# Optimization experiments

Hardware: AMD Instinct MI355X
Metric: run time of the kernel (lower is better)

The kernel has to match this reference:

```python
import jax, jax.numpy as jnp
import numpy as np

B, T, D = 1, 1024, 1024
H = 16; HKV = 16; HD = D // H; R = 2; K = 3; LOWR = 32
HR = HKV * R                      # heads after harmonic expansion
OUTW = HKV * HD * 2 * R           # w_proj output width
SCALE = HD ** -0.5


def setup_inputs() -> dict:
    key = jax.random.key(0)
    ks = jax.random.split(key, 10)
    def rn(k, shape, sc=1.0):
        return jax.random.normal(k, shape, dtype=jnp.float32) * sc
    return {
        'hidden_states': rn(ks[0], (B, T, D)),
        'q_w': rn(ks[1], (D, D), D ** -0.5),
        'k_w': rn(ks[2], (D, D), D ** -0.5),
        'v_w': rn(ks[3], (D, D), D ** -0.5),
        'w1': rn(ks[4], (LOWR, D), D ** -0.5),
        'w2': rn(ks[5], (OUTW, LOWR), LOWR ** -0.5),
        'conv_w': rn(ks[6], (OUTW, K), K ** -0.5),
        'bt_w': rn(ks[7], (HKV * R, D), D ** -0.5),
        'bt_b': jnp.zeros((HKV * R,), jnp.float32),
        'o_w': rn(ks[8], (D, D * R), (D * R) ** -0.5),
        'omega': 0.01 * jnp.ones((1, 1, 1, R), jnp.float32),
        'phi': jnp.zeros((1, 1, 1, R), jnp.float32),
    }


def path_attention_forward(hidden_states, q_w, k_w, v_w, w1, w2, conv_w,
                           bt_w, bt_b, o_w, omega, phi):
    b, t, _ = hidden_states.shape
    q = hidden_states @ q_w.T
    k = hidden_states @ k_w.T
    v = hidden_states @ v_w.T
    # low-rank w projection, causal depthwise short conv (kernel K), SiLU
    w_raw = (hidden_states @ w1.T) @ w2.T                    # [b,t,OUTW]
    xp = jnp.pad(w_raw, ((0, 0), (K - 1, 0), (0, 0)))
    w_raw = sum(xp[:, i:i + t, :] * conv_w[:, i] for i in range(K))
    w_raw = jax.nn.silu(w_raw)
    # rotary-like harmonic mixing of Householder directions
    w5 = w_raw.reshape(b, t, HKV, 2 * R, HD)
    Ah = w5[:, :, :, 0::2, :]                                # [b,t,HKV,R,HD]
    Bh = w5[:, :, :, 1::2, :]
    pos = jnp.arange(t, dtype=jnp.float32)[None, :, None, None]
    theta = omega * pos + phi                                # [1,t,1,R]
    c = jnp.cos(theta)[..., None]
    s = jnp.sin(theta)[..., None]
    Wdir = Ah * c + Bh * s
    Wdir = Wdir * jax.lax.rsqrt(jnp.sum(Wdir * Wdir, -1, keepdims=True) + 1e-6)
    beta = jax.nn.sigmoid(hidden_states @ bt_w.T + bt_b) * 2.0   # [b,t,HR]
    # repeat-interleave q/k/v heads across harmonics -> [b,HR,t,HD]
    to_h = lambda x: jnp.swapaxes(jnp.repeat(x.reshape(b, t, H, HD), R, axis=2), 1, 2)
    qh, kh, vh = to_h(q), to_h(k), to_h(v)
    wh = jnp.swapaxes(Wdir.reshape(b, t, HR, HD), 1, 2)      # [b,HR,t,HD]
    bh = jnp.swapaxes(beta, 1, 2)                            # [b,HR,t]
    # PaTH logits: A_ij = q_i^T (H_i ... H_{j+1}) k_j, H_t = I - beta_t w_t w_t^T.
    # WY/UT transform: with M_ts = beta_t (w_t.w_s) for s<t, the coefficients
    # B_tj (t>j) of the accumulated rank-1 corrections solve the unit-lower
    # triangular system (I + M) B = strilow(Db W K^T), and
    # A = tril(Q K^T - tril(Q W^T) B).
    idx = jnp.arange(t)
    strict = idx[:, None] > idx[None, :]
    incl = idx[:, None] >= idx[None, :]
    Mw = jnp.where(strict, jnp.einsum('bhtd,bhsd->bhts', wh, wh) * bh[..., None], 0.0)
    rhs = jnp.where(strict, jnp.einsum('bhtd,bhjd->bhtj', wh, kh) * bh[..., None], 0.0)
    Bmat = jax.scipy.linalg.solve_triangular(Mw + jnp.eye(t, dtype=Mw.dtype), rhs, lower=True)
    qk = jnp.einsum('bhid,bhjd->bhij', qh, kh)
    qw = jnp.where(incl, jnp.einsum('bhid,bhtd->bhit', qh, wh), 0.0)
    logits = (qk - jnp.einsum('bhit,bhtj->bhij', qw, Bmat)) * SCALE
    logits = jnp.where(incl, logits, -1e30)
    p = jax.nn.softmax(logits, axis=-1)
    o = jnp.einsum('bhij,bhjd->bhid', p, vh)                 # [b,HR,t,HD]
    o = jnp.swapaxes(o, 1, 2).reshape(b, t, HR * HD)         # [b,t,D*R]
    return o @ o_w.T


def reference(hidden_states, q_w, k_w, v_w, w1, w2, conv_w, bt_w, bt_b, o_w, omega, phi):
    return path_attention_forward(hidden_states, q_w, k_w, v_w, w1, w2, conv_w,
                                  bt_w, bt_b, o_w, omega, phi)
```

## Files before the change

### kernel.cpp

```cpp
#include <hip/hip_runtime.h>
#include <math.h>

#define TTD 1024
#define DDM 1024
#define HDIM 64
#define PSC2 0.18033688011112042f
#define LS 72

typedef __attribute__((ext_vector_type(8))) __bf16 bf16x8;
typedef __attribute__((ext_vector_type(4))) float f32x4;
#define MFMA16(a,b,c) __builtin_amdgcn_mfma_f32_16x16x32_bf16(a,b,c,0,0,0)

#define STR_(x) #x
#define WAITVM(N) asm volatile("s_waitcnt vmcnt(" STR_(N) ")" ::: "memory")
#define BAR() do { __builtin_amdgcn_s_barrier(); asm volatile("" ::: "memory"); } while (0)
#define LGKBAR() do { asm volatile("s_waitcnt lgkmcnt(0)" ::: "memory"); \
                      __builtin_amdgcn_s_barrier(); asm volatile("" ::: "memory"); } while (0)
#define FULLBAR() do { asm volatile("s_waitcnt vmcnt(0) lgkmcnt(0)" ::: "memory"); \
                       __builtin_amdgcn_s_barrier(); asm volatile("" ::: "memory"); } while (0)

__device__ __forceinline__ ushort f2b(float f) {
  unsigned u = __builtin_bit_cast(unsigned, f);
  return (ushort)((u + 0x7fffu + ((u >> 16) & 1u)) >> 16);
}
__device__ __forceinline__ float b2f(ushort u) {
  unsigned v = (unsigned)u << 16;
  return __builtin_bit_cast(float, v);
}

__device__ __forceinline__ void gload_lds16(const ushort* g, ushort* l) {
  __builtin_amdgcn_global_load_lds(
      (const __attribute__((address_space(1))) unsigned*)g,
      (__attribute__((address_space(3))) unsigned*)l, 16, 0, 0);
}

#define SWZ(row, cc) (((row) * 8 + ((cc) ^ ((row) & 7))) * 8)
#define SWZE(row, col) (SWZ(row, (col) >> 3) + ((col) & 7))
#define SWZ2(row, cc) (((row) * 8 + ((cc) ^ (((row) & 7) ^ ((row) >> 3)))) * 8)
#define SWZ2E(row, col) (SWZ2(row, (col) >> 3) + ((col) & 7))

__device__ __forceinline__ void stage_tile(const ushort* gb, long gs, ushort* tile,
                                           int w, int l) {
  int sub = l >> 3, cc = (l & 7) ^ sub;
  #pragma unroll
  for (int it = 0; it < 2; ++it) {
    int q = w * 2 + it;
    gload_lds16(gb + (long)(q * 8 + sub) * gs + cc * 8, &tile[(q * 64 + l) * 8]);
  }
}

__device__ __forceinline__ bf16x8 frag(const ushort* tile, int row, int cc) {
  return *(const bf16x8*)&tile[SWZ(row, cc)];
}
__device__ __forceinline__ bf16x8 frag2(const ushort* tile, int row, int cc) {
  return *(const bf16x8*)&tile[SWZ2(row, cc)];
}

#define XT_PERH   557056L
#define OFF_X     0L
#define OFF_PZ    35651584L
#define OFF_HSB   35651584L
#define OFF_QWW   37748736L
#define OFF_KWW   39845888L
#define OFF_VWW   41943040L
#define OFF_W2B   44040192L
#define OFF_WLOWB 44302336L
#define OFF_TB    98566144L
#define OFF_OALL  98566144L
#define OFF_YB    102760448L
#define OFF_OWB   106954752L
#define OFF_WHB   111149056L
#define OFF_QB    115343360L
#define OFF_KB    117440512L
#define OFF_VTB   119537664L
#define OFF_BETA  121634816L
#define OFF_BW64  121765888L
#define OFF_PO    121896960L
#define OFF_PML   138674176L

#define CVT_TOTAL 6488064L
struct CvtSegs {
  const float* src[8];
  ushort* dst[8];
  long cnt[8];
};
__global__ __launch_bounds__(256) void cvt_all_kernel(CvtSegs sg) {
  long e = ((long)blockIdx.x * 256 + threadIdx.x) * 4;
  #pragma unroll
  for (int s = 0; s < 8; ++s) {
    if (e < sg.cnt[s]) {
      float4 f = *(const float4*)(sg.src[s] + e);
      ushort4 o;
      o.x = f2b(f.x); o.y = f2b(f.y); o.z = f2b(f.z); o.w = f2b(f.w);
      *(ushort4*)(sg.dst[s] + e) = o;
      return;
    }
    e -= sg.cnt[s];
  }
}

__global__ __launch_bounds__(256) void qkv_sp_kernel(
    const ushort* __restrict__ hsb,
    const ushort* __restrict__ wq, const ushort* __restrict__ wk, const ushort* __restrict__ wv,
    const ushort* __restrict__ bw, const float* __restrict__ bt_b,
    ushort* __restrict__ cq, ushort* __restrict__ ck, ushort* __restrict__ cv,
    float* __restrict__ beta, ushort* __restrict__ wlowb)
{
  int z = blockIdx.z;
  if (z == 3 && blockIdx.x != 0) return;
  const ushort* B = (z == 0) ? wq : (z == 1) ? wk : (z == 2) ? wv : bw;

  __shared__ ushort Ab[2][8192];
  __shared__ ushort Bb[2][4096];

  int tid = threadIdx.x, w = tid >> 6, l = tid & 63;
  int quad = l >> 4, lane15 = l & 15;
  int rm = blockIdx.y * 128, cn = (z == 3) ? 0 : blockIdx.x * 64;
  const ushort* Ag = hsb + (long)rm * DDM;
  const ushort* Bg = B + (long)cn * DDM;

  stage_tile(Ag, DDM, &Ab[0][0], w, l);
  stage_tile(Ag + 64 * DDM, DDM, &Ab[0][4096], w, l);
  stage_tile(Bg, DDM, &Bb[0][0], w, l);

  f32x4 acc[2][4] = {};
  int arow0 = (w & 1) * 32 + lane15;
  int asel = (w >> 1) * 4096;
  for (int kt = 0; kt < 16; ++kt) {
    int cur = kt & 1;
    if (kt < 15) {
      int nxt = cur ^ 1;
      stage_tile(Ag + (kt + 1) * 64, DDM, &Ab[nxt][0], w, l);
      stage_tile(Ag + 64 * DDM + (kt + 1) * 64, DDM, &Ab[nxt][4096], w, l);
      stage_tile(Bg + (kt + 1) * 64, DDM, &Bb[nxt][0], w, l);
      WAITVM(6);
    } else {
      WAITVM(0);
    }
    BAR();
    const ushort* Atile = &Ab[cur][asel];
    #pragma unroll
    for (int s = 0; s < 2; ++s) {
      bf16x8 a0 = frag(Atile, arow0, s * 4 + quad);
      bf16x8 a1 = frag(Atile, arow0 + 16, s * 4 + quad);
      #pragma unroll
      for (int f = 0; f < 4; ++f) {
        bf16x8 bf = frag(&Bb[cur][0], f * 16 + lane15, s * 4 + quad);
        acc[0][f] = MFMA16(a0, bf, acc[0][f]);
        acc[1][f] = MFMA16(a1, bf, acc[1][f]);
      }
    }
    BAR();
  }

  if (z < 2) {
    ushort* Cb = (z == 0) ? cq : ck;
    #pragma unroll
    for (int rr = 0; rr < 2; ++rr) {
      int orow = rm + w * 32 + rr * 16 + quad * 4;
      #pragma unroll
      for (int f = 0; f < 4; ++f)
        #pragma unroll
        for (int r = 0; r < 4; ++r)
          Cb[(long)(orow + r) * DDM + cn + f * 16 + lane15] = f2b(acc[rr][f][r]);
    }
  } else if (z == 2) {
    #pragma unroll
    for (int rr = 0; rr < 2; ++rr) {
      int orow = rm + w * 32 + rr * 16 + quad * 4;
      #pragma unroll
      for (int f = 0; f < 4; ++f) {
        ushort4 o;
        o.x = f2b(acc[rr][f][0]); o.y = f2b(acc[rr][f][1]);
        o.z = f2b(acc[rr][f][2]); o.w = f2b(acc[rr][f][3]);
        *(ushort4*)&cv[(long)(cn + f * 16 + lane15) * TTD + orow] = o;
      }
    }
  } else {
    #pragma unroll
    for (int rr = 0; rr < 2; ++rr) {
      int orow = rm + w * 32 + rr * 16 + quad * 4;
      #pragma unroll
      for (int f = 0; f < 2; ++f) {
        int hr = f * 16 + lane15;
        float bb = bt_b[hr];
        #pragma unroll
        for (int r = 0; r < 4; ++r)
          beta[(long)hr * TTD + orow + r] = 2.f / (1.f + __expf(-(acc[rr][f][r] + bb)));
      }
      #pragma unroll
      for (int f = 2; f < 4; ++f)
        #pragma unroll
        for (int r = 0; r < 4; ++r)
          wlowb[(long)(orow + r) * 32 + (f - 2) * 16 + lane15] = f2b(acc[rr][f][r]);
    }
  }
}

__global__ __launch_bounds__(256) void wraw_solveA_kernel(
    const ushort* __restrict__ wlowb, const ushort* __restrict__ w2b,
    const float* __restrict__ conv_w, const float* __restrict__ omega,
    const float* __restrict__ phi, const float* __restrict__ beta,
    ushort* __restrict__ whb, ushort* __restrict__ TB, ushort* __restrict__ YB)
{
  int c = blockIdx.x;
  int rm = c * 64;
  int p = blockIdx.y;
  int hkv = p >> 1, r = p & 1;
  int c0 = hkv * 256 + r * 128;

  __shared__ char pool_[65568];
  ushort* As = (ushort*)pool_;
  ushort* Bs = (ushort*)(pool_ + 4096);
  float (*WR)[132] = (float(*)[132])(pool_ + 12288);
  ushort* Wrow = (ushort*)(pool_ + 47136);
  ushort* WT   = (ushort*)(pool_ + 56352);
  float (*Lm)[65] = (float(*)[65])pool_;
  float (*Vf)[65] = (float(*)[65])(pool_ + 16640);
  ushort* Tb = (ushort*)(pool_ + 33280);

  int tid = threadIdx.x, w = tid >> 6, l = tid & 63;
  int quad = l >> 4, lane15 = l & 15;

  {
    int row = tid >> 2, ch = (tid & 3) * 8;
    gload_lds16(wlowb + (long)(rm + row) * 32 + ch, &As[row * 32 + ch]);
    gload_lds16(w2b + (long)(c0 + row) * 32 + ch, &Bs[row * 32 + ch]);
    gload_lds16(w2b + (long)(c0 + 64 + row) * 32 + ch, &Bs[(64 + row) * 32 + ch]);
  }
  {
    int hr2 = tid >> 7, col = tid & 127;
    float acc = 0.f;
    if (rm > 0) {
      long t = rm - 2 + hr2;
      for (int k = 0; k < 32; ++k)
        acc += b2f(wlowb[t * 32 + k]) * b2f(w2b[(long)(c0 + col) * 32 + k]);
    }
    WR[hr2][col] = acc;
  }
  FULLBAR();

  #pragma unroll
  for (int g = 0; g < 2; ++g) {
    f32x4 acc[4] = {};
    bf16x8 af = *(const bf16x8*)&As[(w * 16 + lane15) * 32 + quad * 8];
    #pragma unroll
    for (int f = 0; f < 4; ++f) {
      bf16x8 bf = *(const bf16x8*)&Bs[(g * 64 + f * 16 + lane15) * 32 + quad * 8];
      acc[f] = MFMA16(af, bf, acc[f]);
    }
    #pragma unroll
    for (int f = 0; f < 4; ++f)
      #pragma unroll
      for (int rr = 0; rr < 4; ++rr)
        WR[2 + w * 16 + quad * 4 + rr][g * 64 + f * 16 + lane15] = acc[f][rr];
  }
  LGKBAR();

  {
    float cwa[3], cwb[3];
    #pragma unroll
    for (int i = 0; i < 3; ++i) {
      cwa[i] = conv_w[(long)(c0 + l) * 3 + i];
      cwb[i] = conv_w[(long)(c0 + 64 + l) * 3 + i];
    }
    float om = omega[r], ph = phi[r];
    for (int it = 0; it < 16; ++it) {
      int tl = it * 4 + w;
      int t = rm + tl;
      float a = cwa[0] * WR[tl][l] + cwa[1] * WR[tl + 1][l] + cwa[2] * WR[tl + 2][l];
      float b = cwb[0] * WR[tl][64 + l] + cwb[1] * WR[tl + 1][64 + l] + cwb[2] * WR[tl + 2][64 + l];
      a = a / (1.f + __expf(-a));
      b = b / (1.f + __expf(-b));
      float th = om * (float)t + ph;
      float wd = a * __cosf(th) + b * __sinf(th);
      float ss = wd * wd;
      #pragma unroll
      for (int o = 32; o > 0; o >>= 1) ss += __shfl_xor(ss, o, 64);
      ushort hv = f2b(wd * (1.f / sqrtf(ss + 1e-6f)));
      whb[((long)p * TTD + t) * HDIM + l] = hv;
      Wrow[tl * LS + l] = hv;
      WT[l * LS + tl] = hv;
    }
  }
  LGKBAR();

  const float* bet = beta + (long)p * TTD + rm;
  ushort* TBh = TB + ((long)p * 16 + c) * 4096;
  ushort* YBh = YB + ((long)p * 16 + c) * 4096;

  f32x4 g4[4] = {};
  #pragma unroll
  for (int s = 0; s < 2; ++s) {
    bf16x8 af = *(const bf16x8*)&Wrow[(w * 16 + lane15) * LS + s * 32 + quad * 8];
    #pragma unroll
    for (int f = 0; f < 4; ++f) {
      bf16x8 bf = *(const bf16x8*)&Wrow[(f * 16 + lane15) * LS + s * 32 + quad * 8];
      g4[f] = MFMA16(af, bf, g4[f]);
    }
  }
  #pragma unroll
  for (int r4 = 0; r4 < 4; ++r4) {
    int t = w * 16 + quad * 4 + r4;
    float bv = bet[t];
    #pragma unroll
    for (int f = 0; f < 4; ++f) {
      int tp = f * 16 + lane15;
      Lm[t][tp] = (t > tp) ? bv * g4[f][r4] : 0.f;
    }
  }
  LGKBAR();

  {
    float cur[16];
    #pragma unroll
    for (int i = 0; i < 16; ++i) cur[i] = (w * 16 + i == l) ? bet[l] : 0.f;
    for (int sb = 0; sb < 4; ++sb) {
      if (w == sb) {
        float xloc[16];
        #pragma unroll
        for (int i = 0; i < 16; ++i) {
          float bv = cur[i];
          #pragma unroll
          for (int j2 = 0; j2 < 16; ++j2)
            if (j2 < i) bv -= Lm[sb * 16 + i][sb * 16 + j2] * xloc[j2];
          xloc[i] = bv;
          Vf[sb * 16 + i][l] = bv;
        }
      }
      LGKBAR();
      if (w > sb) {
        float xp[16];
        #pragma unroll
        for (int t = 0; t < 16; ++t) xp[t] = Vf[sb * 16 + t][l];
        #pragma unroll
        for (int i = 0; i < 16; ++i) {
          float s2 = cur[i];
          #pragma unroll
          for (int t = 0; t < 16; ++t) s2 -= Lm[w * 16 + i][sb * 16 + t] * xp[t];
          cur[i] = s2;
        }
      }
    }
  }
  {
    int t = tid >> 2, off = (tid & 3) * 16;
    ushort tmp[16];
    #pragma unroll
    for (int i = 0; i < 16; ++i) { tmp[i] = f2b(Vf[t][off + i]); Tb[t * LS + off + i] = tmp[i]; }
    *(uint4*)&TBh[t * 64 + off] = *(const uint4*)&tmp[0];
    *(uint4*)&TBh[t * 64 + off + 8] = *(const uint4*)&tmp[8];
  }
  LGKBAR();
  f32x4 y[4] = {};
  #pragma unroll
  for (int s = 0; s < 2; ++s) {
    bf16x8 af = *(const bf16x8*)&Tb[(w * 16 + lane15) * LS + s * 32 + quad * 8];
    #pragma unroll
    for (int f = 0; f < 4; ++f) {
      bf16x8 bf = *(const bf16x8*)&WT[(f * 16 + lane15) * LS + s * 32 + quad * 8];
      y[f] = MFMA16(af, bf, y[f]);
    }
  }
  #pragma unroll
  for (int f = 0; f < 4; ++f)
    #pragma unroll
    for (int r4 = 0; r4 < 4; ++r4)
      YBh[(long)(w * 16 + quad * 4 + r4) * 64 + f * 16 + lane15] = f2b(y[f][r4]);
}

__global__ __launch_bounds__(256) void solveB_kernel(
    const ushort* __restrict__ whb, const ushort* __restrict__ kb,
    const ushort* __restrict__ TB, const ushort* __restrict__ YB,
    ushort* __restrict__ Xb, ushort* __restrict__ KZ)
{
  int h = blockIdx.x;
  int ty = blockIdx.y;
  int js = (ty < 8) ? ty : (23 - ty);
  int j0 = js * 64;
  const ushort* wh_h = whb + (long)h * TTD * HDIM;
  const ushort* k_h = kb + (long)(h >> 1) * 64;
  ushort* X_h = Xb + (long)h * XT_PERH;
  ushort* KZ_h = KZ + (long)h * 15 * TTD * HDIM;
  int xidx = js * 16 - js * (js - 1) / 2;

  __shared__ ushort KT[4096];
  __shared__ ushort WT[4096];
  __shared__ ushort XM[4096];
  __shared__ ushort nS[4096];

  int tid = threadIdx.x, w = tid >> 6, l = tid & 63;
  int quad = l >> 4, lane15 = l & 15;
  f32x4 Sacc[4] = {}, Wacc[4] = {};

  stage_tile(k_h + (long)j0 * DDM, DDM, KT, w, l);

  float kreg[4][4];
  #pragma unroll
  for (int f = 0; f < 4; ++f)
    #pragma unroll
    for (int r = 0; r < 4; ++r)
      kreg[f][r] = b2f(k_h[(long)(j0 + w * 16 + quad * 4 + r) * DDM + f * 16 + lane15]);

  int prow0 = tid >> 3, pd0 = (tid & 7) * 8;
  uint4 pk0 = *(const uint4*)&wh_h[((long)js * 64 + prow0) * HDIM + pd0];
  uint4 pk1 = *(const uint4*)&wh_h[((long)js * 64 + 32 + prow0) * HDIM + pd0];
  bf16x8 ybr0 = {}, ybr1 = {};

  WAITVM(0);

  for (int c = js; c < 16; ++c) {
    LGKBAR();
    {
      const ushort* pu0 = (const ushort*)&pk0;
      const ushort* pu1 = (const ushort*)&pk1;
      #pragma unroll
      for (int i = 0; i < 8; ++i) WT[SWZ2E(pd0 + i, prow0)] = pu0[i];
      #pragma unroll
      for (int i = 0; i < 8; ++i) WT[SWZ2E(pd0 + i, 32 + prow0)] = pu1[i];
    }
    if (c < 15) {
      pk0 = *(const uint4*)&wh_h[((long)(c + 1) * 64 + prow0) * HDIM + pd0];
      pk1 = *(const uint4*)&wh_h[((long)(c + 1) * 64 + 32 + prow0) * HDIM + pd0];
    }
    f32x4 xacc[4] = {};
    if (c == js) {
      const ushort* whc = wh_h + (long)c * 64 * HDIM;
      f32x4 m[4] = {};
      #pragma unroll
      for (int s = 0; s < 2; ++s) {
        bf16x8 af = *(const bf16x8*)&whc[(long)(w * 16 + lane15) * HDIM + s * 32 + quad * 8];
        #pragma unroll
        for (int f = 0; f < 4; ++f)
          m[f] = MFMA16(af, frag(KT, f * 16 + lane15, s * 4 + quad), m[f]);
      }
      #pragma unroll
      for (int f = 0; f < 4; ++f)
        #pragma unroll
        for (int r = 0; r < 4; ++r) {
          int t = w * 16 + quad * 4 + r, j = f * 16 + lane15;
          XM[SWZE(j, t)] = (t > j) ? f2b(m[f][r]) : (ushort)0;
        }
      LGKBAR();
      const ushort* TBh = TB + ((long)h * 16 + c) * 4096;
      #pragma unroll
      for (int s = 0; s < 2; ++s) {
        bf16x8 af = *(const bf16x8*)&TBh[(long)(w * 16 + lane15) * 64 + s * 32 + quad * 8];
        #pragma unroll
        for (int f = 0; f < 4; ++f)
          xacc[f] = MFMA16(af, frag(XM, f * 16 + lane15, s * 4 + quad), xacc[f]);
      }
      LGKBAR();
    } else {
      #pragma unroll
      for (int f = 0; f < 4; ++f) {
        xacc[f] = MFMA16(ybr0, frag(KT, f * 16 + lane15, 0 * 4 + quad), xacc[f]);
        xacc[f] = MFMA16(ybr0, frag(nS, f * 16 + lane15, 0 * 4 + quad), xacc[f]);
        xacc[f] = MFMA16(ybr1, frag(KT, f * 16 + lane15, 1 * 4 + quad), xacc[f]);
        xacc[f] = MFMA16(ybr1, frag(nS, f * 16 + lane15, 1 * 4 + quad), xacc[f]);
      }
    }
    #pragma unroll
    for (int f = 0; f < 4; ++f)
      #pragma unroll
      for (int r = 0; r < 4; ++r)
        XM[SWZE(f * 16 + lane15, w * 16 + quad * 4 + r)] = f2b(xacc[f][r]);
    LGKBAR();
    {
      ushort* xt = X_h + (long)xidx * 4096;
      int j = tid >> 2, c2 = (tid & 3) * 2;
      bf16x8 s0 = frag(XM, j, c2);
      bf16x8 s1 = frag(XM, j, c2 + 1);
      *(bf16x8*)&xt[j * 64 + c2 * 8] = s0;
      *(bf16x8*)&xt[j * 64 + c2 * 8 + 8] = s1;
    }
    ++xidx;
    if (c < 15) {
      {
        const ushort* YBn = YB + ((long)h * 16 + c + 1) * 4096;
        ybr0 = *(const bf16x8*)&YBn[(long)(w * 16 + lane15) * 64 + 0 * 32 + quad * 8];
        ybr1 = *(const bf16x8*)&YBn[(long)(w * 16 + lane15) * 64 + 1 * 32 + quad * 8];
      }
      #pragma unroll
      for (int s = 0; s < 2; ++s) {
        bf16x8 aw = frag2(WT, w * 16 + lane15, s * 4 + quad);
        bf16x8 ax = frag(XM, w * 16 + lane15, s * 4 + quad);
        #pragma unroll
        for (int f = 0; f < 4; ++f) {
          Sacc[f] = MFMA16(aw, frag(XM, f * 16 + lane15, s * 4 + quad), Sacc[f]);
          Wacc[f] = MFMA16(ax, frag2(WT, f * 16 + lane15, s * 4 + quad), Wacc[f]);
        }
      }
      ushort* pz = KZ_h + (long)c * TTD * HDIM;
      #pragma unroll
      for (int f = 0; f < 4; ++f)
        #pragma unroll
        for (int r = 0; r < 4; ++r)
          pz[(long)(j0 + w * 16 + quad * 4 + r) * 64 + f * 16 + lane15] =
              f2b(kreg[f][r] - Wacc[f][r]);
      #pragma unroll
      for (int f = 0; f < 4; ++f)
        #pragma unroll
        for (int r = 0; r < 4; ++r)
          nS[SWZE(f * 16 + lane15, w * 16 + quad * 4 + r)] = f2b(-Sacc[f][r]);
    }
  }
}

__global__ __launch_bounds__(256) void flash_kernel(
    const ushort* __restrict__ qb, const ushort* __restrict__ kbuf,
    const ushort* __restrict__ whb, const ushort* __restrict__ Xb,
    const ushort* __restrict__ KZ, const ushort* __restrict__ vTb,
    float* __restrict__ partO, float* __restrict__ partML)
{
  int h = blockIdx.x;
  int y = blockIdx.y;
  int ri = 15 - (y >> 1);
  int half = y & 1;
  int nlo = (ri + 1) >> 1;
  int jb0 = half ? nlo : 0;
  int jb1 = half ? ri : (nlo - 1);
  int r0 = ri * 64;
  const ushort* q_h = qb + (long)(h >> 1) * 64;
  const ushort* k_h = kbuf + (long)(h >> 1) * 64;
  const ushort* wh_h = whb + (long)h * TTD * HDIM;
  const ushort* X_h = Xb + (long)h * XT_PERH;
  const ushort* kz = KZ + ((long)h * 15 + (ri - 1)) * TTD * HDIM;
  const ushort* v_h = vTb + (long)(h >> 1) * 64 * TTD;

  __shared__ ushort S[2][3][4096];
  __shared__ ushort QWD[4096];
  __shared__ ushort PT[4096];

  int tid = threadIdx.x, w = tid >> 6, l = tid & 63;
  int quad = l >> 4, lane15 = l & 15;

  bf16x8 aq[2];
  #pragma unroll
  for (int s = 0; s < 2; ++s)
    aq[s] = *(const bf16x8*)&q_h[(long)(r0 + w * 16 + lane15) * DDM + s * 32 + quad * 8];
  bf16x8 kones;
  #pragma unroll
  for (int i = 0; i < 8; ++i) kones[i] = (__bf16)1.0f;

  long xidx0 = (long)jb0 * 16 - (long)jb0 * (jb0 - 1) / 2 + (ri - jb0);
  const ushort* xst = X_h + xidx0 * 4096;
  if (jb0 <= jb1) {
    if (jb0 == ri) stage_tile(k_h + (long)r0 * DDM, DDM, &S[0][0][0], w, l);
    else           stage_tile(kz + (long)jb0 * 4096, 64, &S[0][0][0], w, l);
    stage_tile(xst, 64, &S[0][1][0], w, l);
    stage_tile(v_h + jb0 * 64, TTD, &S[0][2][0], w, l);
  }
  {
    f32x4 t4[4] = {};
    #pragma unroll
    for (int s = 0; s < 2; ++s)
      #pragma unroll
      for (int f = 0; f < 4; ++f) {
        bf16x8 bf = *(const bf16x8*)&wh_h[(long)(r0 + f * 16 + lane15) * HDIM + s * 32 + quad * 8];
        t4[f] = MFMA16(aq[s], bf, t4[f]);
      }
    #pragma unroll
    for (int f = 0; f < 4; ++f)
      #pragma unroll
      for (int r = 0; r < 4; ++r) {
        int i = w * 16 + quad * 4 + r, t = f * 16 + lane15;
        QWD[SWZE(i, t)] = (i >= t) ? f2b(-t4[f][r]) : (ushort)0;
      }
  }

  f32x4 O[4] = {};
  f32x4 O5 = {};
  float m[4];
  #pragma unroll
  for (int r = 0; r < 4; ++r) m[r] = -1e30f;

  for (int jb = jb0; jb <= jb1; ++jb) {
    int cur = (jb - jb0) & 1;
    const ushort* xnx = xst + (long)(15 - jb) * 4096;
    if (jb < jb1) {
      int jn = jb + 1;
      ushort* nb = &S[cur ^ 1][0][0];
      if (jn < ri) stage_tile(kz + (long)jn * 4096, 64, nb, w, l);
      else         stage_tile(k_h + (long)r0 * DDM, DDM, nb, w, l);
      stage_tile(xnx, 64, nb + 4096, w, l);
      stage_tile(v_h + jn * 64, TTD, nb + 8192, w, l);
      WAITVM(6);
    } else {
      WAITVM(0);
    }
    BAR();
    const ushort* Sb = &S[cur][0][0];
    const ushort* Sx = &S[cur][1][0];
    const ushort* Sv = &S[cur][2][0];
    f32x4 acc[4] = {};
    #pragma unroll
    for (int s = 0; s < 2; ++s)
      #pragma unroll
      for (int f = 0; f < 4; ++f)
        acc[f] = MFMA16(aq[s], frag(Sb, f * 16 + lane15, s * 4 + quad), acc[f]);
    #pragma unroll
    for (int s = 0; s < 2; ++s) {
      bf16x8 aw = frag(QWD, w * 16 + lane15, s * 4 + quad);
      #pragma unroll
      for (int f = 0; f < 4; ++f)
        acc[f] = MFMA16(aw, frag(Sx, f * 16 + lane15, s * 4 + quad), acc[f]);
    }
    float rmax[4] = {-3e38f, -3e38f, -3e38f, -3e38f};
    #pragma unroll
    for (int f = 0; f < 4; ++f)
      #pragma unroll
      for (int r = 0; r < 4; ++r) {
        float lv = acc[f][r] * PSC2;
        if (jb == ri && (f * 16 + lane15) > (w * 16 + quad * 4 + r)) lv = -3e38f;
        acc[f][r] = lv;
        rmax[r] = fmaxf(rmax[r], lv);
      }
    #pragma unroll
    for (int r = 0; r < 4; ++r) {
      rmax[r] = fmaxf(rmax[r], __shfl_xor(rmax[r], 1, 64));
      rmax[r] = fmaxf(rmax[r], __shfl_xor(rmax[r], 2, 64));
      rmax[r] = fmaxf(rmax[r], __shfl_xor(rmax[r], 4, 64));
      rmax[r] = fmaxf(rmax[r], __shfl_xor(rmax[r], 8, 64));
    }
    bool grow = (rmax[0] > m[0]) | (rmax[1] > m[1]) | (rmax[2] > m[2]) | (rmax[3] > m[3]);
    if (__any(grow)) {
      float alpha[4];
      #pragma unroll
      for (int r = 0; r < 4; ++r) {
        float nm = fmaxf(m[r], rmax[r]);
        alpha[r] = exp2f(m[r] - nm);
        m[r] = nm;
        O5[r] *= alpha[r];
      }
      #pragma unroll
      for (int f = 0; f < 4; ++f)
        #pragma unroll
        for (int r = 0; r < 4; ++r) O[f][r] *= alpha[r];
    }
    #pragma unroll
    for (int f = 0; f < 4; ++f)
      #pragma unroll
      for (int r = 0; r < 4; ++r)
        acc[f][r] = exp2f(acc[f][r] - m[r]);
    #pragma unroll
    for (int f = 0; f < 4; ++f)
      #pragma unroll
      for (int r = 0; r < 4; ++r) {
        int i = w * 16 + quad * 4 + r;
        PT[SWZE(i, f * 16 + lane15)] = f2b(acc[f][r]);
      }
    #pragma unroll
    for (int s = 0; s < 2; ++s) {
      bf16x8 ap = frag(PT, w * 16 + lane15, s * 4 + quad);
      #pragma unroll
      for (int f = 0; f < 4; ++f)
        O[f] = MFMA16(ap, frag(Sv, f * 16 + lane15, s * 4 + quad), O[f]);
      O5 = MFMA16(ap, kones, O5);
    }
    BAR();
    xst = xnx;
  }
  long p = ((long)h * 16 + ri) * 2 + half;
  float* PO = partO + p * 4096;
  float* PM = partML + p * 128;
  #pragma unroll
  for (int f = 0; f < 4; ++f)
    #pragma unroll
    for (int r = 0; r < 4; ++r)
      PO[(w * 16 + quad * 4 + r) * 64 + f * 16 + lane15] = O[f][r];
  if (lane15 == 0) {
    #pragma unroll
    for (int r = 0; r < 4; ++r) {
      int i = w * 16 + quad * 4 + r;
      PM[i] = m[r];
      PM[64 + i] = O5[r];
    }
  }
}

__global__ __launch_bounds__(256) void merge_kernel(
    const float* __restrict__ PO, const float* __restrict__ PML,
    ushort* __restrict__ oall)
{
  int h = blockIdx.x, ri = blockIdx.y;
  int r0 = ri * 64;
  long p0 = ((long)h * 16 + ri) * 2;
  int tid = threadIdx.x;
  int row = tid >> 2, c0 = (tid & 3) * 16;
  float m1 = PML[p0 * 128 + row],      l1 = PML[p0 * 128 + 64 + row];
  float m2 = PML[(p0 + 1) * 128 + row], l2 = PML[(p0 + 1) * 128 + 64 + row];
  float M = fmaxf(m1, m2);
  float a1 = exp2f(m1 - M), a2 = exp2f(m2 - M);
  float inv = 1.f / (l1 * a1 + l2 * a2);
  const float* O1 = PO + p0 * 4096 + row * 64 + c0;
  const float* O2 = PO + (p0 + 1) * 4096 + row * 64 + c0;
  ushort* dst = oall + (long)(r0 + row) * 2048 + h * 64 + c0;
  #pragma unroll
  for (int j4 = 0; j4 < 4; ++j4) {
    float4 o1 = *(const float4*)(O1 + j4 * 4);
    float4 o2 = *(const float4*)(O2 + j4 * 4);
    ushort4 o;
    o.x = f2b((o1.x * a1 + o2.x * a2) * inv);
    o.y = f2b((o1.y * a1 + o2.y * a2) * inv);
    o.z = f2b((o1.z * a1 + o2.z * a2) * inv);
    o.w = f2b((o1.w * a1 + o2.w * a2) * inv);
    *(ushort4*)(dst + j4 * 4) = o;
  }
}

__global__ __launch_bounds__(256) void gemm_out_kernel(
    const ushort* __restrict__ A, const ushort* __restrict__ Bb, float* __restrict__ C)
{
  __shared__ ushort Ab[2][8192];
  __shared__ ushort Bt[2][8192];
  int tid = threadIdx.x, w = tid >> 6, l = tid & 63;
  int quad = l >> 4, lane15 = l & 15;
  int rm = blockIdx.y * 64, cn = blockIdx.x * 64;
  const ushort* Ag = A + (long)rm * 2048;
  const ushort* Bg = Bb + (long)cn * 2048;

  stage_tile(Ag, 2048, &Ab[0][0], w, l);
  stage_tile(Ag + 64, 2048, &Ab[0][4096], w, l);
  stage_tile(Bg, 2048, &Bt[0][0], w, l);
  stage_tile(Bg + 64, 2048, &Bt[0][4096], w, l);

  f32x4 acc[4] = {};
  for (int kt = 0; kt < 16; ++kt) {
    int cur = kt & 1;
    if (kt < 15) {
      int nxt = cur ^ 1;
      long o = (long)(kt + 1) * 128;
      stage_tile(Ag + o, 2048, &Ab[nxt][0], w, l);
      stage_tile(Ag + o + 64, 2048, &Ab[nxt][4096], w, l);
      stage_tile(Bg + o, 2048, &Bt[nxt][0], w, l);
      stage_tile(Bg + o + 64, 2048, &Bt[nxt][4096], w, l);
      WAITVM(8);
    } else {
      WAITVM(0);
    }
    BAR();
    #pragma unroll
    for (int u = 0; u < 2; ++u)
      #pragma unroll
      for (int s = 0; s < 2; ++s) {
        bf16x8 af = frag(&Ab[cur][u * 4096], w * 16 + lane15, s * 4 + quad);
        #pragma unroll
        for (int f = 0; f < 4; ++f)
          acc[f] = MFMA16(af, frag(&Bt[cur][u * 4096], f * 16 + lane15, s * 4 + quad), acc[f]);
      }
    BAR();
  }
  int orow = rm + w * 16 + quad * 4;
  #pragma unroll
  for (int f = 0; f < 4; ++f)
    #pragma unroll
    for (int r = 0; r < 4; ++r)
      C[(long)(orow + r) * DDM + cn + f * 16 + lane15] = acc[f][r];
}

extern "C" void kernel_launch(void* const* d_in, const int* in_sizes, int n_in,
                              void* d_out, int out_size, void* d_ws, size_t ws_size,
                              hipStream_t stream) {
  const float* hs     = (const float*)d_in[0];
  const float* q_w    = (const float*)d_in[1];
  const float* k_w    = (const float*)d_in[2];
  const float* v_w    = (const float*)d_in[3];
  const float* w1     = (const float*)d_in[4];
  const float* w2     = (const float*)d_in[5];
  const float* conv_w = (const float*)d_in[6];
  const float* bt_w   = (const float*)d_in[7];
  const float* bt_b   = (const float*)d_in[8];
  const float* o_w    = (const float*)d_in[9];
  const float* omega  = (const float*)d_in[10];
  const float* phi    = (const float*)d_in[11];
  float* out = (float*)d_out;
  char* ws = (char*)d_ws;

  ushort* Xb     = (ushort*)(ws + OFF_X);
  ushort* KZb    = (ushort*)(ws + OFF_PZ);
  ushort* hs_b   = (ushort*)(ws + OFF_HSB);
  ushort* qw_wb  = (ushort*)(ws + OFF_QWW);
  ushort* kw_wb  = (ushort*)(ws + OFF_KWW);
  ushort* vw_wb  = (ushort*)(ws + OFF_VWW);
  ushort* w2_b   = (ushort*)(ws + OFF_W2B);
  ushort* wlow_b = (ushort*)(ws + OFF_WLOWB);
  ushort* TB     = (ushort*)(ws + OFF_TB);
  ushort* o_all  = (ushort*)(ws + OFF_OALL);
  ushort* YB     = (ushort*)(ws + OFF_YB);
  ushort* ow_b   = (ushort*)(ws + OFF_OWB);
  ushort* wh_b   = (ushort*)(ws + OFF_WHB);
  ushort* q_b    = (ushort*)(ws + OFF_QB);
  ushort* k_b    = (ushort*)(ws + OFF_KB);
  ushort* vT_b   = (ushort*)(ws + OFF_VTB);
  float*  beta   = (float*)(ws + OFF_BETA);
  ushort* bw_b   = (ushort*)(ws + OFF_BW64);
  float*  partO  = (float*)(ws + OFF_PO);
  float*  partML = (float*)(ws + OFF_PML);

  CvtSegs sg;
  sg.src[0] = hs;   sg.dst[0] = hs_b;          sg.cnt[0] = 1048576;
  sg.src[1] = q_w;  sg.dst[1] = qw_wb;         sg.cnt[1] = 1048576;
  sg.src[2] = k_w;  sg.dst[2] = kw_wb;         sg.cnt[2] = 1048576;
  sg.src[3] = v_w;  sg.dst[3] = vw_wb;         sg.cnt[3] = 1048576;
  sg.src[4] = w2;   sg.dst[4] = w2_b;          sg.cnt[4] = 131072;
  sg.src[5] = bt_w; sg.dst[5] = bw_b;          sg.cnt[5] = 32768;
  sg.src[6] = w1;   sg.dst[6] = bw_b + 32768;  sg.cnt[6] = 32768;
  sg.src[7] = o_w;  sg.dst[7] = ow_b;          sg.cnt[7] = 2097152;
  cvt_all_kernel<<<dim3((CVT_TOTAL + 1023) / 1024), 256, 0, stream>>>(sg);

  qkv_sp_kernel<<<dim3(16, 8, 4), 256, 0, stream>>>(
      hs_b, qw_wb, kw_wb, vw_wb, bw_b, bt_b, q_b, k_b, vT_b, beta, wlow_b);

  wraw_solveA_kernel<<<dim3(16, 32), 256, 0, stream>>>(
      wlow_b, w2_b, conv_w, omega, phi, beta, wh_b, TB, YB);

  solveB_kernel<<<dim3(32, 16), 256, 0, stream>>>(wh_b, k_b, TB, YB, Xb, KZb);

  flash_kernel<<<dim3(32, 32), 256, 0, stream>>>(
      q_b, k_b, wh_b, Xb, KZb, vT_b, partO, partML);
  merge_kernel<<<dim3(32, 16), 256, 0, stream>>>(partO, partML, o_all);

  gemm_out_kernel<<<dim3(16, 16), 256, 0, stream>>>(o_all, ow_b, out);

  (void)in_sizes; (void)n_in; (void)out_size; (void)ws_size;
}
```

Baseline: 208.7 us.

## Load K/X/V MFMA operands directly from global instead of LDS staging

Removes the double-buffered shared-memory staging of the K, X and V tiles in the flash kernel, along with its waitcnt and barrier synchronisation. MFMA B-operands are now loaded straight from global memory, and the Q·W fragments are hoisted into registers once before the loop. The launch bounds are set to target three blocks per CU. This cuts LDS footprint and barriers to raise occupancy, at the cost of each wave re-reading full tiles from global memory with no explicit prefetch or overlap.

```diff
diff --git a/kernel.cpp b/kernel.cpp
--- a/kernel.cpp
+++ b/kernel.cpp
@@ -507,7 +507,7 @@
   }
 }
 
-__global__ __launch_bounds__(256) void flash_kernel(
+__global__ __launch_bounds__(256, 3) void flash_kernel(
     const ushort* __restrict__ qb, const ushort* __restrict__ kbuf,
     const ushort* __restrict__ whb, const ushort* __restrict__ Xb,
     const ushort* __restrict__ KZ, const ushort* __restrict__ vTb,
@@ -528,12 +528,12 @@
   const ushort* kz = KZ + ((long)h * 15 + (ri - 1)) * TTD * HDIM;
   const ushort* v_h = vTb + (long)(h >> 1) * 64 * TTD;
 
-  __shared__ ushort S[2][3][4096];
   __shared__ ushort QWD[4096];
   __shared__ ushort PT[4096];
 
   int tid = threadIdx.x, w = tid >> 6, l = tid & 63;
   int quad = l >> 4, lane15 = l & 15;
+  int brow = 0;
 
   bf16x8 aq[2];
   #pragma unroll
@@ -543,14 +543,6 @@
   #pragma unroll
   for (int i = 0; i < 8; ++i) kones[i] = (__bf16)1.0f;
 
-  long xidx0 = (long)jb0 * 16 - (long)jb0 * (jb0 - 1) / 2 + (ri - jb0);
-  const ushort* xst = X_h + xidx0 * 4096;
-  if (jb0 <= jb1) {
-    if (jb0 == ri) stage_tile(k_h + (long)r0 * DDM, DDM, &S[0][0][0], w, l);
-    else           stage_tile(kz + (long)jb0 * 4096, 64, &S[0][0][0], w, l);
-    stage_tile(xst, 64, &S[0][1][0], w, l);
-    stage_tile(v_h + jb0 * 64, TTD, &S[0][2][0], w, l);
-  }
   {
     f32x4 t4[4] = {};
     #pragma unroll
@@ -568,6 +560,9 @@
         QWD[SWZE(i, t)] = (i >= t) ? f2b(-t4[f][r]) : (ushort)0;
       }
   }
+  bf16x8 aqw[2];
+  aqw[0] = frag(QWD, w * 16 + lane15, 0 * 4 + quad);
+  aqw[1] = frag(QWD, w * 16 + lane15, 1 * 4 + quad);
 
   f32x4 O[4] = {};
   f32x4 O5 = {};
@@ -575,36 +570,24 @@
   #pragma unroll
   for (int r = 0; r < 4; ++r) m[r] = -1e30f;
 
+  long xoff = ((long)jb0 * 16 - (long)jb0 * (jb0 - 1) / 2 + (ri - jb0)) * 4096;
+  (void)brow;
   for (int jb = jb0; jb <= jb1; ++jb) {
-    int cur = (jb - jb0) & 1;
-    const ushort* xnx = xst + (long)(15 - jb) * 4096;
-    if (jb < jb1) {
-      int jn = jb + 1;
-      ushort* nb = &S[cur ^ 1][0][0];
-      if (jn < ri) stage_tile(kz + (long)jn * 4096, 64, nb, w, l);
-      else         stage_tile(k_h + (long)r0 * DDM, DDM, nb, w, l);
-      stage_tile(xnx, 64, nb + 4096, w, l);
-      stage_tile(v_h + jn * 64, TTD, nb + 8192, w, l);
-      WAITVM(6);
-    } else {
-      WAITVM(0);
-    }
-    BAR();
-    const ushort* Sb = &S[cur][0][0];
-    const ushort* Sx = &S[cur][1][0];
-    const ushort* Sv = &S[cur][2][0];
+    const ushort* xb_ = X_h + xoff;
     f32x4 acc[4] = {};
     #pragma unroll
-    for (int s = 0; s < 2; ++s)
-      #pragma unroll
-      for (int f = 0; f < 4; ++f)
-        acc[f] = MFMA16(aq[s], frag(Sb, f * 16 + lane15, s * 4 + quad), acc[f]);
-    #pragma unroll
     for (int s = 0; s < 2; ++s) {
-      bf16x8 aw = frag(QWD, w * 16 + lane15, s * 4 + quad);
-      #pragma unroll
-      for (int f = 0; f < 4; ++f)
-        acc[f] = MFMA16(aw, frag(Sx, f * 16 + lane15, s * 4 + quad), acc[f]);
+      int co = (s * 4 + quad) * 8;
+      #pragma unroll
+      for (int f = 0; f < 4; ++f) {
+        int row = f * 16 + lane15;
+        bf16x8 bk;
+        if (jb == ri) bk = *(const bf16x8*)&k_h[(long)(r0 + row) * DDM + co];
+        else          bk = *(const bf16x8*)&kz[(long)jb * 4096 + row * 64 + co];
+        bf16x8 bx = *(const bf16x8*)&xb_[row * 64 + co];
+        acc[f] = MFMA16(aq[s], bk, acc[f]);
+        acc[f] = MFMA16(aqw[s], bx, acc[f]);
+      }
     }
     float rmax[4] = {-3e38f, -3e38f, -3e38f, -3e38f};
     #pragma unroll
@@ -652,14 +635,16 @@
       }
     #pragma unroll
     for (int s = 0; s < 2; ++s) {
+      int co = (s * 4 + quad) * 8;
       bf16x8 ap = frag(PT, w * 16 + lane15, s * 4 + quad);
       #pragma unroll
-      for (int f = 0; f < 4; ++f)
-        O[f] = MFMA16(ap, frag(Sv, f * 16 + lane15, s * 4 + quad), O[f]);
+      for (int f = 0; f < 4; ++f) {
+        bf16x8 bv = *(const bf16x8*)&v_h[(long)(f * 16 + lane15) * TTD + jb * 64 + co];
+        O[f] = MFMA16(ap, bv, O[f]);
+      }
       O5 = MFMA16(ap, kones, O5);
     }
-    BAR();
-    xst = xnx;
+    xoff += (long)(15 - jb) * 4096;
   }
   long p = ((long)h * 16 + ri) * 2 + half;
   float* PO = partO + p * 4096;
```

Result: slower. 243.2 us (+16.6%).
